# Kernel tuning notes

Hardware: AMD Instinct MI355X
Metric: run time of the kernel (lower is better)

Reference implementation:

```python
import jax, jax.numpy as jnp
import numpy as np

K = 128      # classes
CIN = 128    # ch_in
CL = 128     # ch_latent
B, H, W = 8, 1, 8192
SLOPE = 0.01 # F.leaky_relu default
EPS = 1e-5   # BatchNorm eps


def lrelu(x):
    return jnp.where(x >= 0, x, SLOPE * x)


def conv1x1(x, w, b):
    # x: (B,C,H,W), w: (O,C), b: (O,)
    return jnp.einsum('bchw,oc->bohw', x, w) + b[None, :, None, None]


def bn_eval(x, gamma, beta, mean, var):
    scale = gamma * jax.lax.rsqrt(var + EPS)
    return x * scale[None, :, None, None] + (beta - mean * scale)[None, :, None, None]


def setup_inputs() -> dict:
    key = jax.random.key(0)
    ks = jax.random.split(key, 16)
    def w(k, shape, fan_in):
        return jax.random.normal(k, shape, jnp.float32) / np.sqrt(fan_in)
    return {
        'x_in': jax.random.normal(ks[0], (B, CIN, H, W), jnp.float32),
        'cl1_w': w(ks[1], (CL, CIN), CIN), 'cl1_b': jnp.zeros((CL,), jnp.float32),
        'bn1_gamma': jnp.ones((CL,), jnp.float32), 'bn1_beta': jnp.zeros((CL,), jnp.float32),
        'bn1_mean': 0.1 * jax.random.normal(ks[2], (CL,), jnp.float32),
        'bn1_var': jax.random.uniform(ks[3], (CL,), jnp.float32, 0.5, 1.5),
        'cl2_w': w(ks[4], (CL, CL), CL), 'cl2_b': jnp.zeros((CL,), jnp.float32),
        'cl3_w': w(ks[5], (K + 1, CL), CL), 'cl3_b': jnp.zeros((K + 1,), jnp.float32),
        'reg1_w': w(ks[6], (CL, CIN), CIN), 'reg1_b': jnp.zeros((CL,), jnp.float32),
        'bnr_gamma': jnp.ones((CL,), jnp.float32), 'bnr_beta': jnp.zeros((CL,), jnp.float32),
        'bnr_mean': 0.1 * jax.random.normal(ks[7], (CL,), jnp.float32),
        'bnr_var': jax.random.uniform(ks[8], (CL,), jnp.float32, 0.5, 1.5),
        'cm2_w': w(ks[9], (K, CL, 32), CL), 'cm2_b': jnp.zeros((K, 32), jnp.float32),
        'cm3_w': w(ks[10], (K, 32, 1), 32), 'cm3_b': jnp.zeros((K, 1), jnp.float32),
    }


def reference(x_in, cl1_w, cl1_b, bn1_gamma, bn1_beta, bn1_mean, bn1_var,
              cl2_w, cl2_b, cl3_w, cl3_b,
              reg1_w, reg1_b, bnr_gamma, bnr_beta, bnr_mean, bnr_var,
              cm2_w, cm2_b, cm3_w, cm3_b):
    # classification branch
    x = lrelu(bn_eval(conv1x1(x_in, cl1_w, cl1_b), bn1_gamma, bn1_beta, bn1_mean, bn1_var))
    x = lrelu(conv1x1(x, cl2_w, cl2_b))
    x = conv1x1(x, cl3_w, cl3_b)                    # (B, K+1, H, W)
    logits = x[:, :K]
    mask = lrelu(x[:, -1:])                          # (B,1,H,W)
    inds = jnp.argmax(logits, axis=1)                # (B,H,W) int
    inds_r = inds.reshape(-1).astype(jnp.int32)      # (N,)
    xr = lrelu(bn_eval(conv1x1(x_in, reg1_w, reg1_b), bnr_gamma, bnr_beta, bnr_mean, bnr_var))
    # torch: transpose(1,3).reshape(-1, C)  -> (B,W,H,C) flatten
    xr = jnp.transpose(xr, (0, 3, 2, 1)).reshape(-1, CL)   # (N, CL)
    # CondMul 1: per-pixel gathered weight (N,CL,32)
    h = lrelu(jnp.einsum('ni,nio->no', xr, cm2_w[inds_r]) + cm2_b[inds_r])
    # CondMul 2: (N,32)->(N,1)
    reg = jnp.einsum('ni,nio->no', h, cm3_w[inds_r]) + cm3_b[inds_r]
    reg = reg.reshape(B, 1, 1, -1)                   # (B,1,1,H*W)
    x_real = (inds[:, None].astype(jnp.float32) + reg) * (1.0 / K)
    return x_real, mask
```

## Files before the change

kernel.cpp:

```cpp
#include <hip/hip_runtime.h>
#include <math.h>

#define NPOS 65536
#define NCH  128
#define DELTA 0.008f
#define HPAD 16

#define OFF_XR   0u
#define OFF_W1T  8388608u
#define OFF_W2T  (OFF_W1T + 16384u)
#define OFF_W3T  (OFF_W2T + 16384u)
#define OFF_B1F  (OFF_W3T + 16384u)
#define OFF_BRF  (OFF_B1F + 128u)
#define OFF_B2F  (OFF_BRF + 128u)
#define OFF_B3F  (OFF_B2F + 128u)
#define OFF_BF16 (OFF_B3F + 132u)
#define OFF_INT  (OFF_BF16 + 329728u)

#define UW1H 0u
#define UW1L 16384u
#define UWRH 32768u
#define UWRL 49152u
#define UW2H 65536u
#define UW2L 81920u
#define UW3H 98304u
#define UW3L 116736u
#define UW2K 135168u

#define NST 2080

typedef short bf16x8 __attribute__((ext_vector_type(8)));
typedef float f32x4 __attribute__((ext_vector_type(4)));
#define MFMA16 __builtin_amdgcn_mfma_f32_16x16x32_bf16

__device__ __forceinline__ float lrelu(float v) { return v >= 0.0f ? v : 0.01f * v; }
__device__ __forceinline__ unsigned short f2bf(float f) {
    unsigned u = __float_as_uint(f);
    return (unsigned short)((u + 0x7fffu + ((u >> 16) & 1u)) >> 16);
}
__device__ __forceinline__ float bf2f(unsigned short h) {
    return __uint_as_float(((unsigned)h) << 16);
}
__device__ __forceinline__ unsigned long long pack4(unsigned short a, unsigned short b,
                                                    unsigned short c, unsigned short d) {
    return (unsigned long long)a | ((unsigned long long)b << 16)
         | ((unsigned long long)c << 32) | ((unsigned long long)d << 48);
}

__global__ void k_prep(const float* __restrict__ cl1_w, const float* __restrict__ cl1_b,
                       const float* __restrict__ g1, const float* __restrict__ be1,
                       const float* __restrict__ mu1, const float* __restrict__ va1,
                       const float* __restrict__ cl2_w, const float* __restrict__ cl2_b,
                       const float* __restrict__ cl3_w, const float* __restrict__ cl3_b,
                       const float* __restrict__ reg1_w, const float* __restrict__ reg1_b,
                       const float* __restrict__ gr, const float* __restrict__ ber,
                       const float* __restrict__ mur, const float* __restrict__ var_,
                       const float* __restrict__ cm2w,
                       float* __restrict__ ws_f, unsigned short* __restrict__ wbf,
                       int* __restrict__ hist, int* __restrict__ fixcnt)
{
    const int bid = blockIdx.x;
    const int t = threadIdx.x;
    if (bid >= 128) {
        __shared__ float tl[32 * 132];
        int k = bid - 128;
        #pragma unroll
        for (int i = 0; i < 32; ++i) {
            float v = cm2w[(unsigned)k * 4096u + i * 128 + t];
            int ci = i * 4 + (t >> 5), o = t & 31;
            tl[o * 132 + ci] = v;
        }
        __syncthreads();
        #pragma unroll
        for (int i = 0; i < 32; ++i)
            wbf[UW2K + (unsigned)k * 4096u + i * 128 + t] = f2bf(tl[i * 132 + t]);
        return;
    }
    int tid = bid * 128 + t;
    int cin = tid >> 7, cout = tid & 127;
    float s1 = g1[cout] / sqrtf(va1[cout] + 1e-5f);
    float sr = gr[cout] / sqrtf(var_[cout] + 1e-5f);
    float w1 = cl1_w[cout * 128 + cin] * s1;
    float wr = reg1_w[cout * 128 + cin] * sr;
    float w2 = cl2_w[cout * 128 + cin];
    float w3 = cl3_w[cout * 128 + cin];
    ws_f[OFF_W1T + tid] = w1;
    ws_f[OFF_W2T + tid] = w2;
    ws_f[OFF_W3T + tid] = w3;
    int j = cout * 128 + cin;
    unsigned short h;
    h = f2bf(w1); wbf[UW1H + j] = h; wbf[UW1L + j] = f2bf(w1 - bf2f(h));
    h = f2bf(wr); wbf[UWRH + j] = h; wbf[UWRL + j] = f2bf(wr - bf2f(h));
    h = f2bf(w2); wbf[UW2H + j] = h; wbf[UW2L + j] = f2bf(w2 - bf2f(h));
    h = f2bf(w3); wbf[UW3H + j] = h; wbf[UW3L + j] = f2bf(w3 - bf2f(h));
    if (tid < 2048) {
        int r = tid >> 7, ci = tid & 127;
        float v = (r == 0) ? cl3_w[128 * 128 + ci] : 0.0f;
        int jj = (128 + r) * 128 + ci;
        h = f2bf(v); wbf[UW3H + jj] = h; wbf[UW3L + jj] = f2bf(v - bf2f(h));
    }
    if (tid < 128) {
        float s1b = g1[tid] / sqrtf(va1[tid] + 1e-5f);
        float srb = gr[tid] / sqrtf(var_[tid] + 1e-5f);
        ws_f[OFF_B1F + tid] = cl1_b[tid] * s1b + be1[tid] - mu1[tid] * s1b;
        ws_f[OFF_BRF + tid] = reg1_b[tid] * srb + ber[tid] - mur[tid] * srb;
        ws_f[OFF_B2F + tid] = cl2_b[tid];
        hist[tid * HPAD] = 0;
    }
    if (tid < 129) ws_f[OFF_B3F + tid] = cl3_b[tid];
    if (tid == 0) fixcnt[0] = 0;
}

__global__ __launch_bounds__(256, 2)
void k_fused(const float* __restrict__ X, const float* __restrict__ wsf,
             const unsigned short* __restrict__ wbf,
             unsigned short* __restrict__ XRB, float* __restrict__ out_mask,
             int* __restrict__ inds, int* __restrict__ fixcnt,
             int* __restrict__ fixlist)
{
    __shared__ __align__(16) unsigned short XBh[64 * 136];
    __shared__ __align__(16) unsigned short XBl[64 * 136];
    __shared__ float sm1[4 * 64];
    __shared__ float sm2[4 * 64];
    __shared__ int   si1[4 * 64];

    const int t = threadIdx.x;
    const int lane = t & 63;
    const int cl16 = lane & 15;
    const int q8 = (lane >> 4) * 8;
    const int q4 = (lane >> 4) * 4;
    const int wv = __builtin_amdgcn_readfirstlane(t >> 6);
    const unsigned nt64 = blockIdx.x * 64u;
    const unsigned base = nt64 + (nt64 >> 13) * 1040384u;

    const unsigned short* W1H = wbf + UW1H; const unsigned short* W1L = wbf + UW1L;
    const unsigned short* WRH = wbf + UWRH; const unsigned short* WRL = wbf + UWRL;
    const unsigned short* W2H = wbf + UW2H; const unsigned short* W2L = wbf + UW2L;
    const unsigned short* W3H = wbf + UW3H; const unsigned short* W3L = wbf + UW3L;
    const float* b1f = wsf + OFF_B1F;
    const float* brf = wsf + OFF_BRF;
    const float* b2f = wsf + OFF_B2F;
    const float* b3f = wsf + OFF_B3F;

    const f32x4 vzero = {0.f, 0.f, 0.f, 0.f};

    {
        const int pos = t & 63, cig = t >> 6;
        #pragma unroll
        for (int l = 0; l < 8; ++l) {
            int ci0 = cig * 32 + l * 4;
            float v0 = X[base + (unsigned)(ci0 + 0) * 8192u + pos];
            float v1 = X[base + (unsigned)(ci0 + 1) * 8192u + pos];
            float v2 = X[base + (unsigned)(ci0 + 2) * 8192u + pos];
            float v3 = X[base + (unsigned)(ci0 + 3) * 8192u + pos];
            unsigned short h0 = f2bf(v0), h1 = f2bf(v1), h2 = f2bf(v2), h3 = f2bf(v3);
            unsigned long long ph = pack4(h0, h1, h2, h3);
            unsigned long long pl = pack4(f2bf(v0 - bf2f(h0)), f2bf(v1 - bf2f(h1)),
                                          f2bf(v2 - bf2f(h2)), f2bf(v3 - bf2f(h3)));
            *(unsigned long long*)&XBh[pos * 136 + ci0] = ph;
            *(unsigned long long*)&XBl[pos * 136 + ci0] = pl;
        }
    }
    __syncthreads();

    f32x4 aY[2][4], aR[2][4];
    #pragma unroll
    for (int m = 0; m < 2; ++m)
        #pragma unroll
        for (int n = 0; n < 4; ++n) { aY[m][n] = vzero; aR[m][n] = vzero; }
    #pragma unroll
    for (int kt = 0; kt < 4; ++kt) {
        bf16x8 Bh[4], Bl[4];
        #pragma unroll
        for (int n = 0; n < 4; ++n) {
            int bo = (n * 16 + cl16) * 136 + kt * 32 + q8;
            Bh[n] = *(const bf16x8*)&XBh[bo];
            Bl[n] = *(const bf16x8*)&XBl[bo];
        }
        #pragma unroll
        for (int m = 0; m < 2; ++m) {
            int ao = (wv * 32 + m * 16 + cl16) * 128 + kt * 32 + q8;
            bf16x8 a1h = *(const bf16x8*)&W1H[ao], a1l = *(const bf16x8*)&W1L[ao];
            bf16x8 arh = *(const bf16x8*)&WRH[ao], arl = *(const bf16x8*)&WRL[ao];
            #pragma unroll
            for (int n = 0; n < 4; ++n) {
                aY[m][n] = MFMA16(a1h, Bl[n], aY[m][n], 0, 0, 0);
                aY[m][n] = MFMA16(a1l, Bh[n], aY[m][n], 0, 0, 0);
                aY[m][n] = MFMA16(a1h, Bh[n], aY[m][n], 0, 0, 0);
                aR[m][n] = MFMA16(arh, Bl[n], aR[m][n], 0, 0, 0);
                aR[m][n] = MFMA16(arl, Bh[n], aR[m][n], 0, 0, 0);
                aR[m][n] = MFMA16(arh, Bh[n], aR[m][n], 0, 0, 0);
            }
        }
    }
    __syncthreads();

    {
        #pragma unroll
        for (int m = 0; m < 2; ++m) {
            int cb = wv * 32 + m * 16 + q4;
            float br0 = brf[cb], br1 = brf[cb + 1], br2 = brf[cb + 2], br3 = brf[cb + 3];
            #pragma unroll
            for (int n = 0; n < 4; ++n) {
                unsigned pb = (nt64 + n * 16 + cl16) * 128u + cb;
                ushort4 xo;
                xo.x = f2bf(lrelu(aR[m][n][0] + br0));
                xo.y = f2bf(lrelu(aR[m][n][1] + br1));
                xo.z = f2bf(lrelu(aR[m][n][2] + br2));
                xo.w = f2bf(lrelu(aR[m][n][3] + br3));
                *(ushort4*)&XRB[pb] = xo;
            }
        }
    }
    {
        #pragma unroll
        for (int m = 0; m < 2; ++m) {
            int cb = wv * 32 + m * 16 + q4;
            float b0 = b1f[cb], b1 = b1f[cb + 1], b2 = b1f[cb + 2], b3 = b1f[cb + 3];
            #pragma unroll
            for (int n = 0; n < 4; ++n) {
                float v0 = lrelu(aY[m][n][0] + b0), v1 = lrelu(aY[m][n][1] + b1);
                float v2 = lrelu(aY[m][n][2] + b2), v3 = lrelu(aY[m][n][3] + b3);
                unsigned short h0 = f2bf(v0), h1 = f2bf(v1), h2 = f2bf(v2), h3 = f2bf(v3);
                unsigned long long ph = pack4(h0, h1, h2, h3);
                unsigned long long pl = pack4(f2bf(v0 - bf2f(h0)), f2bf(v1 - bf2f(h1)),
                                              f2bf(v2 - bf2f(h2)), f2bf(v3 - bf2f(h3)));
                int idx = (n * 16 + cl16) * 136 + cb;
                *(unsigned long long*)&XBh[idx] = ph;
                *(unsigned long long*)&XBl[idx] = pl;
            }
        }
    }
    __syncthreads();

    f32x4 aZ[2][4];
    #pragma unroll
    for (int m = 0; m < 2; ++m)
        #pragma unroll
        for (int n = 0; n < 4; ++n) aZ[m][n] = vzero;
    #pragma unroll
    for (int kt = 0; kt < 4; ++kt) {
        bf16x8 Bh[4], Bl[4];
        #pragma unroll
        for (int n = 0; n < 4; ++n) {
            int bo = (n * 16 + cl16) * 136 + kt * 32 + q8;
            Bh[n] = *(const bf16x8*)&XBh[bo];
            Bl[n] = *(const bf16x8*)&XBl[bo];
        }
        #pragma unroll
        for (int m = 0; m < 2; ++m) {
            int ao = (wv * 32 + m * 16 + cl16) * 128 + kt * 32 + q8;
            bf16x8 ah = *(const bf16x8*)&W2H[ao], al = *(const bf16x8*)&W2L[ao];
            #pragma unroll
            for (int n = 0; n < 4; ++n) {
                aZ[m][n] = MFMA16(ah, Bl[n], aZ[m][n], 0, 0, 0);
                aZ[m][n] = MFMA16(al, Bh[n], aZ[m][n], 0, 0, 0);
                aZ[m][n] = MFMA16(ah, Bh[n], aZ[m][n], 0, 0, 0);
            }
        }
    }
    __syncthreads();
    {
        #pragma unroll
        for (int m = 0; m < 2; ++m) {
            int cb = wv * 32 + m * 16 + q4;
            float b0 = b2f[cb], b1 = b2f[cb + 1], b2 = b2f[cb + 2], b3 = b2f[cb + 3];
            #pragma unroll
            for (int n = 0; n < 4; ++n) {
                float v0 = lrelu(aZ[m][n][0] + b0), v1 = lrelu(aZ[m][n][1] + b1);
                float v2 = lrelu(aZ[m][n][2] + b2), v3 = lrelu(aZ[m][n][3] + b3);
                unsigned short h0 = f2bf(v0), h1 = f2bf(v1), h2 = f2bf(v2), h3 = f2bf(v3);
                unsigned long long ph = pack4(h0, h1, h2, h3);
                unsigned long long pl = pack4(f2bf(v0 - bf2f(h0)), f2bf(v1 - bf2f(h1)),
                                              f2bf(v2 - bf2f(h2)), f2bf(v3 - bf2f(h3)));
                int idx = (n * 16 + cl16) * 136 + cb;
                *(unsigned long long*)&XBh[idx] = ph;
                *(unsigned long long*)&XBl[idx] = pl;
            }
        }
    }
    __syncthreads();

    f32x4 aL[2][4], aM[4];
    #pragma unroll
    for (int m = 0; m < 2; ++m)
        #pragma unroll
        for (int n = 0; n < 4; ++n) aL[m][n] = vzero;
    #pragma unroll
    for (int n = 0; n < 4; ++n) aM[n] = vzero;
    #pragma unroll
    for (int kt = 0; kt < 4; ++kt) {
        bf16x8 Bh[4], Bl[4];
        #pragma unroll
        for (int n = 0; n < 4; ++n) {
            int bo = (n * 16 + cl16) * 136 + kt * 32 + q8;
            Bh[n] = *(const bf16x8*)&XBh[bo];
            Bl[n] = *(const bf16x8*)&XBl[bo];
        }
        #pragma unroll
        for (int m = 0; m < 2; ++m) {
            int ao = (wv * 32 + m * 16 + cl16) * 128 + kt * 32 + q8;
            bf16x8 ah = *(const bf16x8*)&W3H[ao], al = *(const bf16x8*)&W3L[ao];
            #pragma unroll
            for (int n = 0; n < 4; ++n) {
                aL[m][n] = MFMA16(ah, Bl[n], aL[m][n], 0, 0, 0);
                aL[m][n] = MFMA16(al, Bh[n], aL[m][n], 0, 0, 0);
                aL[m][n] = MFMA16(ah, Bh[n], aL[m][n], 0, 0, 0);
            }
        }
        if (wv == 3) {
            int ao = (128 + cl16) * 128 + kt * 32 + q8;
            bf16x8 ah = *(const bf16x8*)&W3H[ao], al = *(const bf16x8*)&W3L[ao];
            #pragma unroll
            for (int n = 0; n < 4; ++n) {
                aM[n] = MFMA16(ah, Bl[n], aM[n], 0, 0, 0);
                aM[n] = MFMA16(al, Bh[n], aM[n], 0, 0, 0);
                aM[n] = MFMA16(ah, Bh[n], aM[n], 0, 0, 0);
            }
        }
    }

    {
        float bb[2][4];
        #pragma unroll
        for (int m = 0; m < 2; ++m) {
            int cb = wv * 32 + m * 16 + q4;
            bb[m][0] = b3f[cb]; bb[m][1] = b3f[cb + 1];
            bb[m][2] = b3f[cb + 2]; bb[m][3] = b3f[cb + 3];
        }
        float m1[4], m2[4]; int i1[4];
        #pragma unroll
        for (int n = 0; n < 4; ++n) {
            m1[n] = -1e30f; m2[n] = -1e30f; i1[n] = 0;
            #pragma unroll
            for (int m = 0; m < 2; ++m) {
                int cb = wv * 32 + m * 16 + q4;
                #pragma unroll
                for (int r = 0; r < 4; ++r) {
                    float v = aL[m][n][r] + bb[m][r];
                    if (v > m1[n]) { m2[n] = m1[n]; m1[n] = v; i1[n] = cb + r; }
                    else if (v > m2[n]) m2[n] = v;
                }
            }
        }
        #pragma unroll
        for (int off = 16; off <= 32; off <<= 1) {
            #pragma unroll
            for (int n = 0; n < 4; ++n) {
                float om1 = __shfl_xor(m1[n], off);
                float om2 = __shfl_xor(m2[n], off);
                int   oi1 = __shfl_xor(i1[n], off);
                if (om1 > m1[n] || (om1 == m1[n] && oi1 < i1[n])) {
                    m2[n] = fmaxf(m1[n], om2); m1[n] = om1; i1[n] = oi1;
                } else {
                    m2[n] = fmaxf(m2[n], om1);
                }
            }
        }
        if ((lane >> 4) == 0) {
            #pragma unroll
            for (int n = 0; n < 4; ++n) {
                sm1[wv * 64 + n * 16 + cl16] = m1[n];
                sm2[wv * 64 + n * 16 + cl16] = m2[n];
                si1[wv * 64 + n * 16 + cl16] = i1[n];
            }
        }
    }
    if (wv == 3 && (lane >> 4) == 0) {
        float mb = b3f[128];
        #pragma unroll
        for (int n = 0; n < 4; ++n)
            out_mask[nt64 + n * 16 + cl16] = lrelu(aM[n][0] + mb);
    }
    __syncthreads();
    if (t < 64) {
        float m1 = sm1[t], m2 = sm2[t];
        int i1 = si1[t];
        #pragma unroll
        for (int w = 1; w < 4; ++w) {
            float v1 = sm1[w * 64 + t];
            float v2 = sm2[w * 64 + t];
            int   vi = si1[w * 64 + t];
            if (v1 > m1) { m2 = fmaxf(m1, v2); m1 = v1; i1 = vi; }
            else         { m2 = fmaxf(m2, v1); }
        }
        int n = nt64 + t;
        inds[n] = i1;
        if (m1 - m2 < DELTA) {
            int slot = atomicAdd(fixcnt, 1);
            fixlist[slot] = n;
        }
    }
}

__global__ __launch_bounds__(256, 4)
void k_fix(const float* __restrict__ X, const float* __restrict__ wsf,
           const int* __restrict__ fixcnt, const int* __restrict__ fixlist,
           int* __restrict__ inds)
{
    const int cnt = fixcnt[0];
    const int t = threadIdx.x;
    const int lane = t & 63;
    const int wv = t >> 6;
    const float* W1T = wsf + OFF_W1T;
    const float* W2T = wsf + OFF_W2T;
    const float* W3T = wsf + OFF_W3T;
    const float* b1f = wsf + OFF_B1F;
    const float* b2f = wsf + OFF_B2F;
    const float* b3f = wsf + OFF_B3F;

    for (int idx = blockIdx.x * 4 + wv; idx < cnt; idx += 1024) {
        int n = fixlist[idx];
        const float* xb = X + (unsigned)(n >> 13) * 1048576u + (unsigned)(n & 8191);
        float x0 = xb[(unsigned)lane * 8192u];
        float x1 = xb[(unsigned)(64 + lane) * 8192u];
        float a0, a1;
        a0 = 0.f; a1 = 0.f;
        for (int ci = 0; ci < 64; ++ci) {
            float xv = __shfl(x0, ci);
            const float* wr = W1T + ci * 128;
            a0 = fmaf(wr[lane], xv, a0);
            a1 = fmaf(wr[64 + lane], xv, a1);
        }
        for (int ci = 0; ci < 64; ++ci) {
            float xv = __shfl(x1, ci);
            const float* wr = W1T + (64 + ci) * 128;
            a0 = fmaf(wr[lane], xv, a0);
            a1 = fmaf(wr[64 + lane], xv, a1);
        }
        x0 = lrelu(a0 + b1f[lane]); x1 = lrelu(a1 + b1f[64 + lane]);
        a0 = 0.f; a1 = 0.f;
        for (int ci = 0; ci < 64; ++ci) {
            float xv = __shfl(x0, ci);
            const float* wr = W2T + ci * 128;
            a0 = fmaf(wr[lane], xv, a0);
            a1 = fmaf(wr[64 + lane], xv, a1);
        }
        for (int ci = 0; ci < 64; ++ci) {
            float xv = __shfl(x1, ci);
            const float* wr = W2T + (64 + ci) * 128;
            a0 = fmaf(wr[lane], xv, a0);
            a1 = fmaf(wr[64 + lane], xv, a1);
        }
        x0 = lrelu(a0 + b2f[lane]); x1 = lrelu(a1 + b2f[64 + lane]);
        a0 = 0.f; a1 = 0.f;
        for (int ci = 0; ci < 64; ++ci) {
            float xv = __shfl(x0, ci);
            const float* wr = W3T + ci * 128;
            a0 = fmaf(wr[lane], xv, a0);
            a1 = fmaf(wr[64 + lane], xv, a1);
        }
        for (int ci = 0; ci < 64; ++ci) {
            float xv = __shfl(x1, ci);
            const float* wr = W3T + (64 + ci) * 128;
            a0 = fmaf(wr[lane], xv, a0);
            a1 = fmaf(wr[64 + lane], xv, a1);
        }
        float L0 = a0 + b3f[lane], L1 = a1 + b3f[64 + lane];
        float v; int id;
        if (L0 >= L1) { v = L0; id = lane; } else { v = L1; id = 64 + lane; }
        #pragma unroll
        for (int off = 1; off < 64; off <<= 1) {
            float ov = __shfl_xor(v, off);
            int   oi = __shfl_xor(id, off);
            if (ov > v || (ov == v && oi < id)) { v = ov; id = oi; }
        }
        if (lane == 0) inds[n] = id;
    }
}

__global__ void k_hist(const int* __restrict__ inds, int* __restrict__ hist)
{
    __shared__ int lh[128];
    int t = threadIdx.x;
    if (t < 128) lh[t] = 0;
    __syncthreads();
    atomicAdd(&lh[inds[blockIdx.x * 256 + t]], 1);
    __syncthreads();
    if (t < 128 && lh[t] > 0) atomicAdd(&hist[t * HPAD], lh[t]);
}

__global__ void k_scan(const int* __restrict__ hist, int* __restrict__ off,
                       int* __restrict__ cur, int* __restrict__ tiles,
                       int* __restrict__ ntt)
{
    __shared__ int s[128];
    __shared__ int s2[128];
    int t = threadIdx.x;
    int v = hist[t * HPAD];
    int ntk = (v + 63) >> 6;
    s[t] = v;
    s2[t] = ntk;
    __syncthreads();
    for (int d = 1; d < 128; d <<= 1) {
        int a  = (t >= d) ? s[t - d]  : 0;
        int a2 = (t >= d) ? s2[t - d] : 0;
        __syncthreads();
        s[t] += a;
        s2[t] += a2;
        __syncthreads();
    }
    off[t] = s[t] - v;
    cur[t * HPAD] = s[t] - v;
    int tb = s2[t] - ntk;
    for (int j = 0; j < ntk; ++j)
        tiles[tb + j] = (t << 16) | j;
    if (t == 127) ntt[0] = s2[127];
}

__global__ void k_scatter(const int* __restrict__ inds, int* __restrict__ cur,
                          int* __restrict__ bucket)
{
    __shared__ int lh[128];
    __shared__ int gb[128];
    int t = threadIdx.x;
    if (t < 128) lh[t] = 0;
    __syncthreads();
    int n = blockIdx.x * 256 + t;
    int id = inds[n];
    int r = atomicAdd(&lh[id], 1);
    __syncthreads();
    if (t < 128 && lh[t] > 0) gb[t] = atomicAdd(&cur[t * HPAD], lh[t]);
    __syncthreads();
    bucket[gb[id] + r] = n;
}

__global__ __launch_bounds__(256, 4)
void k_reg(const unsigned short* __restrict__ XRB, const unsigned short* __restrict__ wbf,
           const float* __restrict__ cm2b, const float* __restrict__ cm3w,
           const float* __restrict__ cm3b, const int* __restrict__ hist,
           const int* __restrict__ off, const int* __restrict__ bucket,
           const int* __restrict__ tiles, const int* __restrict__ ntt,
           float* __restrict__ out)
{
    __shared__ __align__(16) unsigned short XP[4 * NST];
    __shared__ float red[64];
    int bid = blockIdx.x;
    if (bid >= ntt[0]) return;
    int desc = tiles[bid];
    int k = desc >> 16;
    int start = (desc & 0xffff) << 6;
    int cnt = hist[k * HPAD];
    int base = off[k];
    int t = threadIdx.x;
    int lane = t & 63;
    int wv = __builtin_amdgcn_readfirstlane(t >> 6);
    const int n16 = lane & 15;
    const int quad = lane >> 4;

    {
        int rs = t >> 2;
        int q = t & 3;
        int sidx = start + rs;
        if (sidx >= cnt) sidx = cnt - 1;
        int n = bucket[base + sidx];
        const uint4* src = (const uint4*)(XRB + (unsigned)n * 128u + q * 32);
        uint4 a0 = src[0], a1 = src[1], a2 = src[2], a3 = src[3];
        unsigned db = (rs >> 4) * NST + q * 512 + (rs & 15) * 8;
        *(uint4*)&XP[db]       = a0;
        *(uint4*)&XP[db + 128] = a1;
        *(uint4*)&XP[db + 256] = a2;
        *(uint4*)&XP[db + 384] = a3;
    }
    __syncthreads();

    const unsigned short* wb = wbf + UW2K + (unsigned)k * 4096u;
    bf16x8 Bf[2][4];
    #pragma unroll
    for (int nf = 0; nf < 2; ++nf)
        #pragma unroll
        for (int kt = 0; kt < 4; ++kt)
            Bf[nf][kt] = *(const bf16x8*)&wb[(nf * 16 + n16) * 128 + kt * 32 + quad * 8];

    const f32x4 vzero = {0.f, 0.f, 0.f, 0.f};
    f32x4 acc[2];
    acc[0] = vzero; acc[1] = vzero;
    #pragma unroll
    for (int kt = 0; kt < 4; ++kt) {
        bf16x8 Af = *(const bf16x8*)&XP[wv * NST + kt * 512 + lane * 8];
        #pragma unroll
        for (int nf = 0; nf < 2; ++nf)
            acc[nf] = MFMA16(Af, Bf[nf][kt], acc[nf], 0, 0, 0);
    }

    float b2a = cm2b[k * 32 + n16], b2b = cm2b[k * 32 + 16 + n16];
    float w3a = cm3w[k * 32 + n16], w3b = cm3w[k * 32 + 16 + n16];
    #pragma unroll
    for (int r = 0; r < 4; ++r) {
        float p = lrelu(acc[0][r] + b2a) * w3a
                + lrelu(acc[1][r] + b2b) * w3b;
        p += __shfl_xor(p, 1);
        p += __shfl_xor(p, 2);
        p += __shfl_xor(p, 4);
        p += __shfl_xor(p, 8);
        if (n16 == 0)
            red[wv * 16 + quad * 4 + r] = p;
    }
    __syncthreads();
    if (t < 64 && start + t < cnt) {
        int n2 = bucket[base + start + t];
        out[n2] = ((float)k + red[t] + cm3b[k]) * (1.0f / 128.0f);
    }
}

extern "C" void kernel_launch(void* const* d_in, const int* in_sizes, int n_in,
                              void* d_out, int out_size, void* d_ws, size_t ws_size,
                              hipStream_t stream)
{
    (void)in_sizes; (void)n_in; (void)out_size; (void)ws_size;
    const float* x_in   = (const float*)d_in[0];
    const float* cl1_w  = (const float*)d_in[1];
    const float* cl1_b  = (const float*)d_in[2];
    const float* g1     = (const float*)d_in[3];
    const float* be1    = (const float*)d_in[4];
    const float* mu1    = (const float*)d_in[5];
    const float* va1    = (const float*)d_in[6];
    const float* cl2_w  = (const float*)d_in[7];
    const float* cl2_b  = (const float*)d_in[8];
    const float* cl3_w  = (const float*)d_in[9];
    const float* cl3_b  = (const float*)d_in[10];
    const float* reg1_w = (const float*)d_in[11];
    const float* reg1_b = (const float*)d_in[12];
    const float* gr     = (const float*)d_in[13];
    const float* ber    = (const float*)d_in[14];
    const float* mur    = (const float*)d_in[15];
    const float* var_   = (const float*)d_in[16];
    const float* cm2w   = (const float*)d_in[17];
    const float* cm2b   = (const float*)d_in[18];
    const float* cm3w   = (const float*)d_in[19];
    const float* cm3b   = (const float*)d_in[20];

    float* ws_f = (float*)d_ws;
    unsigned short* XRB = (unsigned short*)(ws_f + OFF_XR);
    unsigned short* wbf = (unsigned short*)(ws_f + OFF_BF16);
    int*   wsi    = (int*)(ws_f + OFF_INT);
    int*   inds   = wsi;
    int*   hist   = inds + 65536;
    int*   offb   = hist + 2048;
    int*   cur    = offb + 128;
    int*   ntt    = cur + 2048;
    int*   fixcnt = ntt + 4;
    int*   tiles  = fixcnt + 4;
    int*   fixlist= tiles + 1536;
    int*   bucket = fixlist + 65536;
    float* out = (float*)d_out;

    hipLaunchKernelGGL(k_prep, dim3(256), dim3(128), 0, stream,
                       cl1_w, cl1_b, g1, be1, mu1, va1, cl2_w, cl2_b, cl3_w, cl3_b,
                       reg1_w, reg1_b, gr, ber, mur, var_, cm2w, ws_f, wbf, hist, fixcnt);
    hipLaunchKernelGGL(k_fused, dim3(1024), dim3(256), 0, stream,
                       x_in, ws_f, wbf, XRB, out + 65536, inds, fixcnt, fixlist);
    hipLaunchKernelGGL(k_fix, dim3(256), dim3(256), 0, stream,
                       x_in, ws_f, fixcnt, fixlist, inds);
    hipLaunchKernelGGL(k_hist, dim3(256), dim3(256), 0, stream, inds, hist);
    hipLaunchKernelGGL(k_scan, dim3(1), dim3(128), 0, stream,
                       hist, offb, cur, tiles, ntt);
    hipLaunchKernelGGL(k_scatter, dim3(256), dim3(256), 0, stream, inds, cur, bucket);
    hipLaunchKernelGGL(k_reg, dim3(1536), dim3(256), 0, stream,
                       XRB, wbf, cm2b, cm3w, cm3b, hist, offb, bucket, tiles, ntt, out);
}
```

Baseline: 232.6 us.

## Split fused dual GEMM to cut accumulator registers and raise occupancy

Splits the combined layer-1/regression GEMM into two sequential passes that share one accumulator array, so fewer accumulator registers are live at once. The launch bound goes from 2 to 4 blocks per SM to use the freed registers. The mask-channel MFMA work, previously done only by wave 3 over all four column tiles, is now spread so each wave computes one tile. The cost is a second pass of LDS B-fragment loads for the split GEMM, and the tighter register budget may cause spills.

```diff
diff --git a/kernel.cpp b/kernel.cpp
--- a/kernel.cpp
+++ b/kernel.cpp
@@ -111,7 +111,7 @@
     if (tid == 0) fixcnt[0] = 0;
 }
 
-__global__ __launch_bounds__(256, 2)
+__global__ __launch_bounds__(256, 4)
 void k_fused(const float* __restrict__ X, const float* __restrict__ wsf,
              const unsigned short* __restrict__ wbf,
              unsigned short* __restrict__ XRB, float* __restrict__ out_mask,
@@ -163,11 +163,12 @@
     }
     __syncthreads();
 
-    f32x4 aY[2][4], aR[2][4];
+    f32x4 acc[2][4];
+
     #pragma unroll
     for (int m = 0; m < 2; ++m)
         #pragma unroll
-        for (int n = 0; n < 4; ++n) { aY[m][n] = vzero; aR[m][n] = vzero; }
+        for (int n = 0; n < 4; ++n) acc[m][n] = vzero;
     #pragma unroll
     for (int kt = 0; kt < 4; ++kt) {
         bf16x8 Bh[4], Bl[4];
@@ -180,21 +181,15 @@
         #pragma unroll
         for (int m = 0; m < 2; ++m) {
             int ao = (wv * 32 + m * 16 + cl16) * 128 + kt * 32 + q8;
-            bf16x8 a1h = *(const bf16x8*)&W1H[ao], a1l = *(const bf16x8*)&W1L[ao];
             bf16x8 arh = *(const bf16x8*)&WRH[ao], arl = *(const bf16x8*)&WRL[ao];
             #pragma unroll
             for (int n = 0; n < 4; ++n) {
-                aY[m][n] = MFMA16(a1h, Bl[n], aY[m][n], 0, 0, 0);
-                aY[m][n] = MFMA16(a1l, Bh[n], aY[m][n], 0, 0, 0);
-                aY[m][n] = MFMA16(a1h, Bh[n], aY[m][n], 0, 0, 0);
-                aR[m][n] = MFMA16(arh, Bl[n], aR[m][n], 0, 0, 0);
-                aR[m][n] = MFMA16(arl, Bh[n], aR[m][n], 0, 0, 0);
-                aR[m][n] = MFMA16(arh, Bh[n], aR[m][n], 0, 0, 0);
-            }
-        }
-    }
-    __syncthreads();
-
+                acc[m][n] = MFMA16(arh, Bl[n], acc[m][n], 0, 0, 0);
+                acc[m][n] = MFMA16(arl, Bh[n], acc[m][n], 0, 0, 0);
+                acc[m][n] = MFMA16(arh, Bh[n], acc[m][n], 0, 0, 0);
+            }
+        }
+    }
     {
         #pragma unroll
         for (int m = 0; m < 2; ++m) {
@@ -204,14 +199,41 @@
             for (int n = 0; n < 4; ++n) {
                 unsigned pb = (nt64 + n * 16 + cl16) * 128u + cb;
                 ushort4 xo;
-                xo.x = f2bf(lrelu(aR[m][n][0] + br0));
-                xo.y = f2bf(lrelu(aR[m][n][1] + br1));
-                xo.z = f2bf(lrelu(aR[m][n][2] + br2));
-                xo.w = f2bf(lrelu(aR[m][n][3] + br3));
+                xo.x = f2bf(lrelu(acc[m][n][0] + br0));
+                xo.y = f2bf(lrelu(acc[m][n][1] + br1));
+                xo.z = f2bf(lrelu(acc[m][n][2] + br2));
+                xo.w = f2bf(lrelu(acc[m][n][3] + br3));
                 *(ushort4*)&XRB[pb] = xo;
             }
         }
     }
+
+    #pragma unroll
+    for (int m = 0; m < 2; ++m)
+        #pragma unroll
+        for (int n = 0; n < 4; ++n) acc[m][n] = vzero;
+    #pragma unroll
+    for (int kt = 0; kt < 4; ++kt) {
+        bf16x8 Bh[4], Bl[4];
+        #pragma unroll
+        for (int n = 0; n < 4; ++n) {
+            int bo = (n * 16 + cl16) * 136 + kt * 32 + q8;
+            Bh[n] = *(const bf16x8*)&XBh[bo];
+            Bl[n] = *(const bf16x8*)&XBl[bo];
+        }
+        #pragma unroll
+        for (int m = 0; m < 2; ++m) {
+            int ao = (wv * 32 + m * 16 + cl16) * 128 + kt * 32 + q8;
+            bf16x8 a1h = *(const bf16x8*)&W1H[ao], a1l = *(const bf16x8*)&W1L[ao];
+            #pragma unroll
+            for (int n = 0; n < 4; ++n) {
+                acc[m][n] = MFMA16(a1h, Bl[n], acc[m][n], 0, 0, 0);
+                acc[m][n] = MFMA16(a1l, Bh[n], acc[m][n], 0, 0, 0);
+                acc[m][n] = MFMA16(a1h, Bh[n], acc[m][n], 0, 0, 0);
+            }
+        }
+    }
+    __syncthreads();
     {
         #pragma unroll
         for (int m = 0; m < 2; ++m) {
@@ -219,8 +241,8 @@
             float b0 = b1f[cb], b1 = b1f[cb + 1], b2 = b1f[cb + 2], b3 = b1f[cb + 3];
             #pragma unroll
             for (int n = 0; n < 4; ++n) {
-                float v0 = lrelu(aY[m][n][0] + b0), v1 = lrelu(aY[m][n][1] + b1);
-                float v2 = lrelu(aY[m][n][2] + b2), v3 = lrelu(aY[m][n][3] + b3);
+                float v0 = lrelu(acc[m][n][0] + b0), v1 = lrelu(acc[m][n][1] + b1);
+                float v2 = lrelu(acc[m][n][2] + b2), v3 = lrelu(acc[m][n][3] + b3);
                 unsigned short h0 = f2bf(v0), h1 = f2bf(v1), h2 = f2bf(v2), h3 = f2bf(v3);
                 unsigned long long ph = pack4(h0, h1, h2, h3);
                 unsigned long long pl = pack4(f2bf(v0 - bf2f(h0)), f2bf(v1 - bf2f(h1)),
@@ -233,11 +255,10 @@
     }
     __syncthreads();
 
-    f32x4 aZ[2][4];
     #pragma unroll
     for (int m = 0; m < 2; ++m)
         #pragma unroll
-        for (int n = 0; n < 4; ++n) aZ[m][n] = vzero;
+        for (int n = 0; n < 4; ++n) acc[m][n] = vzero;
     #pragma unroll
     for (int kt = 0; kt < 4; ++kt) {
         bf16x8 Bh[4], Bl[4];
@@ -253,9 +274,9 @@
             bf16x8 ah = *(const bf16x8*)&W2H[ao], al = *(const bf16x8*)&W2L[ao];
             #pragma unroll
             for (int n = 0; n < 4; ++n) {
-                aZ[m][n] = MFMA16(ah, Bl[n], aZ[m][n], 0, 0, 0);
-                aZ[m][n] = MFMA16(al, Bh[n], aZ[m][n], 0, 0, 0);
-                aZ[m][n] = MFMA16(ah, Bh[n], aZ[m][n], 0, 0, 0);
+                acc[m][n] = MFMA16(ah, Bl[n], acc[m][n], 0, 0, 0);
+                acc[m][n] = MFMA16(al, Bh[n], acc[m][n], 0, 0, 0);
+                acc[m][n] = MFMA16(ah, Bh[n], acc[m][n], 0, 0, 0);
             }
         }
     }
@@ -267,8 +288,8 @@
             float b0 = b2f[cb], b1 = b2f[cb + 1], b2 = b2f[cb + 2], b3 = b2f[cb + 3];
             #pragma unroll
             for (int n = 0; n < 4; ++n) {
-                float v0 = lrelu(aZ[m][n][0] + b0), v1 = lrelu(aZ[m][n][1] + b1);
-                float v2 = lrelu(aZ[m][n][2] + b2), v3 = lrelu(aZ[m][n][3] + b3);
+                float v0 = lrelu(acc[m][n][0] + b0), v1 = lrelu(acc[m][n][1] + b1);
+                float v2 = lrelu(acc[m][n][2] + b2), v3 = lrelu(acc[m][n][3] + b3);
                 unsigned short h0 = f2bf(v0), h1 = f2bf(v1), h2 = f2bf(v2), h3 = f2bf(v3);
                 unsigned long long ph = pack4(h0, h1, h2, h3);
                 unsigned long long pl = pack4(f2bf(v0 - bf2f(h0)), f2bf(v1 - bf2f(h1)),
@@ -281,13 +302,11 @@
     }
     __syncthreads();
 
-    f32x4 aL[2][4], aM[4];
+    f32x4 accM = vzero;
     #pragma unroll
     for (int m = 0; m < 2; ++m)
         #pragma unroll
-        for (int n = 0; n < 4; ++n) aL[m][n] = vzero;
-    #pragma unroll
-    for (int n = 0; n < 4; ++n) aM[n] = vzero;
+        for (int n = 0; n < 4; ++n) acc[m][n] = vzero;
     #pragma unroll
     for (int kt = 0; kt < 4; ++kt) {
         bf16x8 Bh[4], Bl[4];
@@ -303,20 +322,17 @@
             bf16x8 ah = *(const bf16x8*)&W3H[ao], al = *(const bf16x8*)&W3L[ao];
             #pragma unroll
             for (int n = 0; n < 4; ++n) {
-                aL[m][n] = MFMA16(ah, Bl[n], aL[m][n], 0, 0, 0);
-                aL[m][n] = MFMA16(al, Bh[n], aL[m][n], 0, 0, 0);
-                aL[m][n] = MFMA16(ah, Bh[n], aL[m][n], 0, 0, 0);
-            }
-        }
-        if (wv == 3) {
+                acc[m][n] = MFMA16(ah, Bl[n], acc[m][n], 0, 0, 0);
+                acc[m][n] = MFMA16(al, Bh[n], acc[m][n], 0, 0, 0);
+                acc[m][n] = MFMA16(ah, Bh[n], acc[m][n], 0, 0, 0);
+            }
+        }
+        {
             int ao = (128 + cl16) * 128 + kt * 32 + q8;
             bf16x8 ah = *(const bf16x8*)&W3H[ao], al = *(const bf16x8*)&W3L[ao];
-            #pragma unroll
-            for (int n = 0; n < 4; ++n) {
-                aM[n] = MFMA16(ah, Bl[n], aM[n], 0, 0, 0);
-                aM[n] = MFMA16(al, Bh[n], aM[n], 0, 0, 0);
-                aM[n] = MFMA16(ah, Bh[n], aM[n], 0, 0, 0);
-            }
+            accM = MFMA16(ah, Bl[wv], accM, 0, 0, 0);
+            accM = MFMA16(al, Bh[wv], accM, 0, 0, 0);
+            accM = MFMA16(ah, Bh[wv], accM, 0, 0, 0);
         }
     }
 
@@ -337,7 +353,7 @@
                 int cb = wv * 32 + m * 16 + q4;
                 #pragma unroll
                 for (int r = 0; r < 4; ++r) {
-                    float v = aL[m][n][r] + bb[m][r];
+                    float v = acc[m][n][r] + bb[m][r];
                     if (v > m1[n]) { m2[n] = m1[n]; m1[n] = v; i1[n] = cb + r; }
                     else if (v > m2[n]) m2[n] = v;
                 }
@@ -366,11 +382,9 @@
             }
         }
     }
-    if (wv == 3 && (lane >> 4) == 0) {
+    if ((lane >> 4) == 0) {
         float mb = b3f[128];
-        #pragma unroll
-        for (int n = 0; n < 4; ++n)
-            out_mask[nt64 + n * 16 + cl16] = lrelu(aM[n][0] + mb);
+        out_mask[nt64 + wv * 16 + cl16] = lrelu(accM[0] + mb);
     }
     __syncthreads();
     if (t < 64) {
```

New measurement: 260.4 us. 1.12x slower.
